# Kernel tuning notes

Hardware: AMD Instinct MI355X
Metric: run time of the kernel (lower is better)

The kernel has to match this reference:

```python
import jax, jax.numpy as jnp
import numpy as np

L, N, E, H, D, F = 2048, 2, 1024, 16, 64, 4096  # seq, batch, embed, heads, head_dim, ffn
EPS = 1e-5


def _ln(x, w, b):
    m = jnp.mean(x, axis=-1, keepdims=True)
    v = jnp.mean(jnp.square(x - m), axis=-1, keepdims=True)
    return (x - m) * jax.lax.rsqrt(v + EPS) * w + b


def setup_inputs() -> dict:
    key = jax.random.key(0)
    ks = jax.random.split(key, 16)
    s = 0.02
    f32 = jnp.float32
    return {
        "x": jax.random.normal(ks[0], (L, N, E), f32),
        "ln1_w": jnp.ones((E,), f32),
        "ln1_b": jnp.zeros((E,), f32),
        "wq": jax.random.normal(ks[1], (H * D, E), f32) * s,
        "bq": jnp.zeros((H * D,), f32),
        "wk": jax.random.normal(ks[2], (H * D, E), f32) * s,
        "bk": jnp.zeros((H * D,), f32),
        "wv": jax.random.normal(ks[3], (H * D, E), f32) * s,
        "bv": jnp.zeros((H * D,), f32),
        "wout": jax.random.normal(ks[4], (E, H * D), f32) * s,
        "bout": jnp.zeros((E,), f32),
        "ln2_w": jnp.ones((E,), f32),
        "ln2_b": jnp.zeros((E,), f32),
        "fc1_w": jax.random.normal(ks[5], (F, E), f32) * s,
        "fc1_b": jnp.zeros((F,), f32),
        "fc2_w": jax.random.normal(ks[6], (E, F), f32) * s,
        "fc2_b": jnp.zeros((E,), f32),
    }


def reference(x, ln1_w, ln1_b, wq, bq, wk, bk, wv, bv, wout, bout,
              ln2_w, ln2_b, fc1_w, fc1_b, fc2_w, fc2_b):
    scale = D ** (-0.5)
    residual = x
    h = _ln(x, ln1_w, ln1_b)                      # (L,N,E)
    q = (h @ wq.T + bq).reshape(L, N, H, D) * scale
    k = (h @ wk.T + bk).reshape(L, N, H, D)
    v = (h @ wv.T + bv).reshape(L, N, H, D)
    attn = jnp.einsum('qnhd,knhd->nhqk', q, k)    # (N,H,L,L) full score matrix
    causal = jnp.tril(jnp.ones((L, L), bool))
    attn = jnp.where(causal[None, None], attn, jnp.float32(-10000.0))
    p = jax.nn.softmax(attn, axis=-1)
    o = jnp.einsum('nhqk,knhd->qnhd', p, v).reshape(L, N, H * D)
    o = o @ wout.T + bout
    x = o + residual
    residual = x
    h = _ln(x, ln2_w, ln2_b)
    h = jax.nn.gelu(h @ fc1_w.T + fc1_b, approximate=False)
    h = h @ fc2_w.T + fc2_b
    return h + residual
```

## Files before the change

### kernel.cpp

```cpp
#include <hip/hip_runtime.h>
#include <hip/hip_bf16.h>
#include <math.h>

using bf16 = __hip_bfloat16;
typedef __bf16 bf16x8 __attribute__((ext_vector_type(8)));
typedef short  short4v __attribute__((ext_vector_type(4)));
typedef float  f32x4  __attribute__((ext_vector_type(4)));

static constexpr int Lq = 2048, Nb = 2, E = 1024, Hh = 16, Dd = 64, Ff = 4096;
static constexpr int MT = Lq * Nb;

__device__ __forceinline__ void async_lds16(const void* g, void* l) {
  __builtin_amdgcn_global_load_lds(
      (const __attribute__((address_space(1))) void*)g,
      (__attribute__((address_space(3))) void*)l, 16, 0, 0);
}
__device__ __forceinline__ bf16x8 ld8(const bf16* p) { return *(const bf16x8*)p; }
__device__ __forceinline__ short bfbits(float x) {
  bf16 t = __float2bfloat16(x);
  return *(short*)&t;
}
__device__ __forceinline__ float gelu_fast(float v) {
  const float y = fminf(2.302208f * (v + 0.044715f * v * v * v), 80.f);
  const float t = exp2f(y);
  return v * t / (t + 1.0f);
}

__global__ __launch_bounds__(256) void cvt_all_kernel(
    const float* __restrict__ wq, const float* __restrict__ wk,
    const float* __restrict__ wv, const float* __restrict__ wout,
    const float* __restrict__ fc1w, const float* __restrict__ fc2w,
    bf16* __restrict__ wqkvb, bf16* __restrict__ woutb,
    bf16* __restrict__ f1wb, bf16* __restrict__ f2wb) {
  const int i = blockIdx.x * 256 + threadIdx.x;
  const float* src;
  bf16* dst;
  size_t off;
  if (i < 786432) {
    const int r = i >> 18;
    off = (size_t)(i & 262143);
    src = (r == 0) ? wq : (r == 1) ? wk : wv;
    dst = wqkvb + (size_t)r * (E * E);
  } else if (i < 1048576) {
    off = (size_t)(i - 786432); src = wout; dst = woutb;
  } else if (i < 2097152) {
    off = (size_t)(i - 1048576); src = fc1w; dst = f1wb;
  } else {
    off = (size_t)(i - 2097152); src = fc2w; dst = f2wb;
  }
  float4 v = ((const float4*)src)[off];
  bf16 o4[4] = {__float2bfloat16(v.x), __float2bfloat16(v.y),
                __float2bfloat16(v.z), __float2bfloat16(v.w)};
  *(uint2*)(dst + 4 * off) = *(uint2*)o4;
}

template <int K, int KSTR, int NOUT, int EPI>
__global__ __launch_bounds__(512, 4) void gemm_tlp(
    const bf16* __restrict__ A, const bf16* __restrict__ W,
    const float* __restrict__ b1, const float* __restrict__ b2,
    const float* __restrict__ b3, float qscale,
    bf16* __restrict__ o0, bf16* __restrict__ o1,
    bf16* __restrict__ o2, bf16* __restrict__ o3) {
  __shared__ __align__(16) bf16 sm[2][12288];
  constexpr int NKT = K / 32;
  static_assert(NKT >= 2, "need >=2 K-tiles");
  const int tid = threadIdx.x;
  const int w = tid >> 6, lane = tid & 63;
  const int quad = lane >> 4, l16 = lane & 15;
  const int wm = (w >> 2) * 64, wn = (w & 3) * 64;
  const int m0 = blockIdx.y * 128, n0 = blockIdx.x * 256;
  const int koff = blockIdx.z * K;

  const int srow = tid >> 2;
  const int sca = ((tid & 3) ^ ((srow >> 1) & 3)) * 8;
  const bf16* Asrc = A + (size_t)(m0 + srow) * KSTR + koff + sca;
  const bf16* Wsrc0 = W + (size_t)(n0 + srow) * KSTR + koff + sca;
  const bf16* Wsrc1 = W + (size_t)(n0 + 128 + srow) * KSTR + koff + sca;
  const int d8 = tid * 8;

  const int kq = ((quad ^ ((l16 >> 1) & 3)) << 3);

  f32x4 acc[4][4];
#pragma unroll
  for (int i = 0; i < 4; i++)
#pragma unroll
    for (int j = 0; j < 4; j++)
#pragma unroll
      for (int r = 0; r < 4; r++) acc[i][j][r] = 0.f;

  async_lds16(Asrc, &sm[0][d8]);
  async_lds16(Wsrc0, &sm[0][4096 + d8]);
  async_lds16(Wsrc1, &sm[0][8192 + d8]);

  for (int kt = 0; kt < NKT; ++kt) {
    const bf16* S = sm[kt & 1];
    if (kt + 1 < NKT) {
      const int kn = (kt + 1) * 32;
      bf16* D = sm[(kt & 1) ^ 1];
      async_lds16(Asrc + kn, &D[d8]);
      async_lds16(Wsrc0 + kn, &D[4096 + d8]);
      async_lds16(Wsrc1 + kn, &D[8192 + d8]);
      asm volatile("s_waitcnt vmcnt(3)" ::: "memory");
    } else {
      asm volatile("s_waitcnt vmcnt(0)" ::: "memory");
    }
    __builtin_amdgcn_s_barrier();

    bf16x8 a[4], b[4];
#pragma unroll
    for (int i = 0; i < 4; i++)
      a[i] = ld8(&S[(wm + i * 16 + l16) * 32 + kq]);
#pragma unroll
    for (int j = 0; j < 4; j++)
      b[j] = ld8(&S[4096 + (wn + j * 16 + l16) * 32 + kq]);

    __builtin_amdgcn_s_setprio(1);
#pragma unroll
    for (int i = 0; i < 4; i++)
#pragma unroll
      for (int j = 0; j < 4; j++)
        acc[i][j] = __builtin_amdgcn_mfma_f32_16x16x32_bf16(a[i], b[j], acc[i][j], 0, 0, 0);
    __builtin_amdgcn_s_setprio(0);
    __builtin_amdgcn_sched_barrier(0);
    __builtin_amdgcn_s_barrier();
  }

  if constexpr (EPI == 2) {
#pragma unroll
    for (int j = 0; j < 4; j++) {
      const int col = n0 + wn + j * 16 + l16;
      const float bv = b1[col];
#pragma unroll
      for (int i = 0; i < 4; i++) {
        const int row = m0 + wm + i * 16 + quad * 4;
#pragma unroll
        for (int r = 0; r < 4; r++) {
          o0[(size_t)(row + r) * NOUT + col] =
              __float2bfloat16(gelu_fast(acc[i][j][r] + bv));
        }
      }
    }
  } else if constexpr (EPI == 3) {
    bf16* dst = (blockIdx.z == 0) ? o0
              : (blockIdx.z == 1) ? o1
              : (blockIdx.z == 2) ? o2 : o3;
#pragma unroll
    for (int j = 0; j < 4; j++) {
      const int col = n0 + wn + j * 16 + l16;
#pragma unroll
      for (int i = 0; i < 4; i++) {
        const int row = m0 + wm + i * 16 + quad * 4;
#pragma unroll
        for (int r = 0; r < 4; r++) {
          dst[(size_t)(row + r) * NOUT + col] = __float2bfloat16(acc[i][j][r]);
        }
      }
    }
  } else {
    const int seg = n0 >> 10;
#pragma unroll
    for (int j = 0; j < 4; j++) {
      const int col = n0 + wn + j * 16 + l16;
      const float bv = (seg == 0) ? b1[col]
                     : (seg == 1) ? b2[col - 1024] : b3[col - 2048];
      const int d = col & 63;
#pragma unroll
      for (int i = 0; i < 4; i++) {
        const int row = m0 + wm + i * 16 + quad * 4;
#pragma unroll
        for (int r = 0; r < 4; r++) {
          const int tok = row + r, n = tok & 1, l = tok >> 1;
          float v = acc[i][j][r] + bv;
          if (seg == 0) {
            o0[(size_t)tok * 1024 + col] = __float2bfloat16(v * qscale);
          } else if (seg == 1) {
            const int h = (col - 1024) >> 6, hh = n * 16 + h;
            o2[((((size_t)hh * 32 + (l >> 6)) * 8 + (d >> 3)) * 64 + (l & 63)) * 8 +
               (d & 7)] = __float2bfloat16(v);
          } else {
            const int h = (col - 2048) >> 6, hh = n * 16 + h;
            o1[((((size_t)hh * 32 + (l >> 6)) * 8 + ((l >> 3) & 7)) * 64 + d) * 8 +
               (l & 7)] = __float2bfloat16(v);
          }
        }
      }
    }
  }
}

__global__ __launch_bounds__(256) void reduce4_kernel(
    const bf16* __restrict__ P0, const bf16* __restrict__ P1,
    const bf16* __restrict__ P2, const bf16* __restrict__ P3,
    const float* __restrict__ bias, float* __restrict__ out) {
  const int i = blockIdx.x * 256 + threadIdx.x;
  const size_t e0 = (size_t)i * 4;
  const int col = (int)(e0 & (E - 1));
  uint2 a0 = *(const uint2*)(P0 + e0);
  uint2 a1 = *(const uint2*)(P1 + e0);
  uint2 a2 = *(const uint2*)(P2 + e0);
  uint2 a3 = *(const uint2*)(P3 + e0);
  const bf16* q0 = (const bf16*)&a0;
  const bf16* q1 = (const bf16*)&a1;
  const bf16* q2 = (const bf16*)&a2;
  const bf16* q3 = (const bf16*)&a3;
  float4 b = *(const float4*)(bias + col);
  float4 r = *(const float4*)(out + e0);
  float4 o;
  o.x = (float)q0[0] + (float)q1[0] + (float)q2[0] + (float)q3[0] + b.x + r.x;
  o.y = (float)q0[1] + (float)q1[1] + (float)q2[1] + (float)q3[1] + b.y + r.y;
  o.z = (float)q0[2] + (float)q1[2] + (float)q2[2] + (float)q3[2] + b.z + r.z;
  o.w = (float)q0[3] + (float)q1[3] + (float)q2[3] + (float)q3[3] + b.w + r.w;
  *(float4*)(out + e0) = o;
}

__global__ __launch_bounds__(256) void redln_kernel(
    const bf16* __restrict__ P, const float* __restrict__ bias,
    const float* __restrict__ res, const float* __restrict__ wgt,
    const float* __restrict__ bia, float* __restrict__ resout,
    bf16* __restrict__ h2) {
  const int t = blockIdx.x, tid = threadIdx.x;
  const size_t base = (size_t)t * E;
  const int e0 = tid * 4;
  uint2 u0 = *(const uint2*)(P + base + e0);
  uint2 u1 = *(const uint2*)(P + (size_t)MT * E + base + e0);
  const bf16* p0 = (const bf16*)&u0;
  const bf16* p1 = (const bf16*)&u1;
  float4 b = *(const float4*)(bias + e0);
  float4 r = *(const float4*)(res + base + e0);
  float v4[4];
  v4[0] = (float)p0[0] + (float)p1[0] + b.x + r.x;
  v4[1] = (float)p0[1] + (float)p1[1] + b.y + r.y;
  v4[2] = (float)p0[2] + (float)p1[2] + b.z + r.z;
  v4[3] = (float)p0[3] + (float)p1[3] + b.w + r.w;
  *(float4*)(resout + base + e0) = *(float4*)v4;

  float s = 0.f, ss = 0.f;
#pragma unroll
  for (int i = 0; i < 4; i++) { s += v4[i]; ss += v4[i] * v4[i]; }
  for (int off = 32; off > 0; off >>= 1) {
    s += __shfl_down(s, off, 64);
    ss += __shfl_down(ss, off, 64);
  }
  __shared__ float rs[4], rss[4], mv[2];
  const int w = tid >> 6;
  if ((tid & 63) == 0) { rs[w] = s; rss[w] = ss; }
  __syncthreads();
  if (tid == 0) {
    float S = rs[0] + rs[1] + rs[2] + rs[3];
    float SS = rss[0] + rss[1] + rss[2] + rss[3];
    float mean = S * (1.f / E);
    float var = SS * (1.f / E) - mean * mean;
    mv[0] = mean; mv[1] = rsqrtf(var + 1e-5f);
  }
  __syncthreads();
  const float mean = mv[0], rstd = mv[1];
  float4 wg = *(const float4*)(wgt + e0);
  float4 bb = *(const float4*)(bia + e0);
  bf16 o4[4];
  o4[0] = __float2bfloat16((v4[0] - mean) * rstd * wg.x + bb.x);
  o4[1] = __float2bfloat16((v4[1] - mean) * rstd * wg.y + bb.y);
  o4[2] = __float2bfloat16((v4[2] - mean) * rstd * wg.z + bb.z);
  o4[3] = __float2bfloat16((v4[3] - mean) * rstd * wg.w + bb.w);
  *(uint2*)(h2 + base + e0) = *(uint2*)o4;
}

__global__ __launch_bounds__(256) void ln_kernel(
    const float* __restrict__ x, const float* __restrict__ wgt,
    const float* __restrict__ bia, bf16* __restrict__ out) {
  const int t = blockIdx.x, tid = threadIdx.x;
  const size_t base = (size_t)t * E;
  float v4[4], s = 0.f, ss = 0.f;
#pragma unroll
  for (int i = 0; i < 4; i++) {
    float v = x[base + i * 256 + tid];
    v4[i] = v; s += v; ss += v * v;
  }
  for (int off = 32; off > 0; off >>= 1) {
    s += __shfl_down(s, off, 64);
    ss += __shfl_down(ss, off, 64);
  }
  __shared__ float rs[4], rss[4], mv[2];
  const int w = tid >> 6;
  if ((tid & 63) == 0) { rs[w] = s; rss[w] = ss; }
  __syncthreads();
  if (tid == 0) {
    float S = rs[0] + rs[1] + rs[2] + rs[3];
    float SS = rss[0] + rss[1] + rss[2] + rss[3];
    float mean = S * (1.f / E);
    float var = SS * (1.f / E) - mean * mean;
    mv[0] = mean; mv[1] = rsqrtf(var + 1e-5f);
  }
  __syncthreads();
  const float mean = mv[0], rstd = mv[1];
#pragma unroll
  for (int i = 0; i < 4; i++) {
    const int e = i * 256 + tid;
    float r = (v4[i] - mean) * rstd * wgt[e] + bia[e];
    out[base + e] = __float2bfloat16(r);
  }
}

__global__ __launch_bounds__(256) void attn_kernel(
    const bf16* __restrict__ Q1, const bf16* __restrict__ KT,
    const bf16* __restrict__ VT, bf16* __restrict__ O) {
  __shared__ __align__(16) bf16 KB[2][512 * 8];
  __shared__ __align__(16) bf16 VB[2][512 * 8];
  const int tid = threadIdx.x;
  const int w = tid >> 6, lane = tid & 63, quad = lane >> 4, l16 = lane & 15;
  const int bid = blockIdx.x;
  const int x = bid & 7;
  const int m = (bid >> 3) & 31;
  const int g = bid >> 8;
  const int j = m >> 2;
  const int hh = (m & 3) * 8 + x;
  const int qt = (g == 0) ? j : (g == 1) ? (31 - j) : (g == 2) ? (j + 8) : (23 - j);
  const int n = hh >> 4, h = hh & 15;

  const bf16* Qp = Q1 + n * E + h * Dd;
  const bf16* Kb = KT + (size_t)hh * 32 * 4096;
  const bf16* Vb = VT + (size_t)hh * 32 * 4096;
  const int so = w * 512 + lane * 8;

  const int ql = qt * 64 + w * 16 + l16;
  const bf16x8 aq0 = ld8(Qp + (size_t)ql * 2048 + quad * 8);
  const bf16x8 aq1 = ld8(Qp + (size_t)ql * 2048 + 32 + quad * 8);
  asm volatile("s_waitcnt vmcnt(0)" ::: "memory");

  async_lds16(Kb + so, &KB[0][w * 512]);
  async_lds16(Kb + 2048 + so, &KB[0][2048 + w * 512]);
  async_lds16(Vb + so, &VB[0][w * 512]);
  async_lds16(Vb + 2048 + so, &VB[0][2048 + w * 512]);

  f32x4 o_acc[4];
#pragma unroll
  for (int d = 0; d < 4; d++)
#pragma unroll
    for (int r = 0; r < 4; r++) o_acc[d][r] = 0.f;
  float m_run = -3e30f, l_run = 0.f;

  for (int kt = 0; kt <= qt; ++kt) {
    const bf16* KBb = KB[kt & 1];
    const bf16* VBb = VB[kt & 1];
    if (kt < qt) {
      const size_t tb = (size_t)(kt + 1) * 4096;
      bf16* Kd = &KB[(kt & 1) ^ 1][0];
      bf16* Vd = &VB[(kt & 1) ^ 1][0];
      async_lds16(Kb + tb + so, Kd + w * 512);
      async_lds16(Kb + tb + 2048 + so, Kd + 2048 + w * 512);
      async_lds16(Vb + tb + so, Vd + w * 512);
      async_lds16(Vb + tb + 2048 + so, Vd + 2048 + w * 512);
      asm volatile("s_waitcnt vmcnt(4)" ::: "memory");
    } else {
      asm volatile("s_waitcnt vmcnt(0)" ::: "memory");
    }
    __builtin_amdgcn_s_barrier();

    f32x4 s[4];
    __builtin_amdgcn_s_setprio(1);
#pragma unroll
    for (int ks = 0; ks < 4; ks++) {
      const bf16x8 kc0 = ld8(&KBb[(size_t)((quad)*64 + ks * 16 + l16) * 8]);
      const bf16x8 kc1 = ld8(&KBb[(size_t)((4 + quad) * 64 + ks * 16 + l16) * 8]);
#pragma unroll
      for (int r = 0; r < 4; r++) s[ks][r] = 0.f;
      s[ks] = __builtin_amdgcn_mfma_f32_16x16x32_bf16(kc0, aq0, s[ks], 0, 0, 0);
      s[ks] = __builtin_amdgcn_mfma_f32_16x16x32_bf16(kc1, aq1, s[ks], 0, 0, 0);
    }
    __builtin_amdgcn_s_setprio(0);

    if (kt == qt) {
#pragma unroll
      for (int ks = 0; ks < 4; ks++) {
#pragma unroll
        for (int r = 0; r < 4; r++) {
          const int kg = kt * 64 + ks * 16 + quad * 4 + r;
          if (kg > ql) s[ks][r] = -14427.0f;
        }
      }
    }

    float tmax = s[0][0];
#pragma unroll
    for (int ks = 0; ks < 4; ks++)
#pragma unroll
      for (int r = 0; r < 4; r++) tmax = fmaxf(tmax, s[ks][r]);
    tmax = fmaxf(tmax, __shfl_xor(tmax, 16, 64));
    tmax = fmaxf(tmax, __shfl_xor(tmax, 32, 64));
    float mbase = m_run;
    if (__any(tmax - m_run > 8.0f)) {
      const float mnew = fmaxf(m_run, tmax);
      const float alpha = exp2f(m_run - mnew);
      m_run = mnew;
      mbase = mnew;
      l_run *= alpha;
#pragma unroll
      for (int d = 0; d < 4; d++)
#pragma unroll
        for (int r = 0; r < 4; r++) o_acc[d][r] *= alpha;
    }
    float rsum = 0.f;
    short4v pf[4];
#pragma unroll
    for (int ks = 0; ks < 4; ks++) {
#pragma unroll
      for (int r = 0; r < 4; r++) {
        const float pv = exp2f(s[ks][r] - mbase);
        rsum += pv;
        pf[ks][r] = bfbits(pv);
      }
    }
    rsum += __shfl_xor(rsum, 16, 64);
    rsum += __shfl_xor(rsum, 32, 64);
    l_run += rsum;

    __builtin_amdgcn_s_setprio(1);
#pragma unroll
    for (int d = 0; d < 4; d++) {
#pragma unroll
      for (int ks = 0; ks < 4; ks++) {
        const int gg = ks * 2 + (quad >> 1);
        const short4v av =
            *(const short4v*)&VBb[(size_t)(gg * 64 + d * 16 + l16) * 8 + (quad & 1) * 4];
        o_acc[d] = __builtin_amdgcn_mfma_f32_16x16x16bf16_1k(av, pf[ks], o_acc[d], 0, 0, 0);
      }
    }
    __builtin_amdgcn_s_setprio(0);

    __builtin_amdgcn_sched_barrier(0);
    __builtin_amdgcn_s_barrier();
  }

  const float inv_l = 1.f / fmaxf(l_run, 1e-30f);
  const size_t obase = (size_t)ql * (Nb * E) + (size_t)n * E + h * Dd;
#pragma unroll
  for (int d = 0; d < 4; d++)
#pragma unroll
    for (int r = 0; r < 4; r++)
      O[obase + d * 16 + quad * 4 + r] = __float2bfloat16(o_acc[d][r] * inv_l);
}

extern "C" void kernel_launch(void* const* d_in, const int* in_sizes, int n_in,
                              void* d_out, int out_size, void* d_ws, size_t ws_size,
                              hipStream_t stream) {
  const float* x    = (const float*)d_in[0];
  const float* ln1w = (const float*)d_in[1];
  const float* ln1b = (const float*)d_in[2];
  const float* wq   = (const float*)d_in[3];
  const float* bq   = (const float*)d_in[4];
  const float* wk   = (const float*)d_in[5];
  const float* bk   = (const float*)d_in[6];
  const float* wv   = (const float*)d_in[7];
  const float* bv   = (const float*)d_in[8];
  const float* wout = (const float*)d_in[9];
  const float* bout = (const float*)d_in[10];
  const float* ln2w = (const float*)d_in[11];
  const float* ln2b = (const float*)d_in[12];
  const float* fc1w = (const float*)d_in[13];
  const float* fc1b = (const float*)d_in[14];
  const float* fc2w = (const float*)d_in[15];
  const float* fc2b = (const float*)d_in[16];

  char* ws = (char*)d_ws;
  bf16* wqkvb = (bf16*)(ws);
  bf16* woutb = (bf16*)(ws + ((size_t)6 << 20));
  bf16* f1wb  = (bf16*)(ws + ((size_t)8 << 20));
  bf16* f2wb  = (bf16*)(ws + ((size_t)16 << 20));
  bf16* h1    = (bf16*)(ws + ((size_t)24 << 20));
  bf16* qk1   = (bf16*)(ws + ((size_t)32 << 20));
  bf16* ktg   = (bf16*)(ws + ((size_t)40 << 20));
  bf16* vtg   = (bf16*)(ws + ((size_t)48 << 20));
  bf16* o     = (bf16*)(ws + ((size_t)56 << 20));
  bf16* Pout  = (bf16*)(ws + ((size_t)32 << 20));
  bf16* f1    = (bf16*)(ws + ((size_t)32 << 20));
  bf16* h2    = h1;
  bf16* FP0   = (bf16*)(ws);
  bf16* FP1   = (bf16*)(ws + ((size_t)8 << 20));
  bf16* FP2   = (bf16*)(ws + ((size_t)64 << 20));
  bf16* FP3   = (bf16*)(ws + ((size_t)72 << 20));
  float* outp = (float*)d_out;

  cvt_all_kernel<<<12288, 256, 0, stream>>>(wq, wk, wv, wout, fc1w, fc2w,
                                            wqkvb, woutb, f1wb, f2wb);

  ln_kernel<<<MT, 256, 0, stream>>>(x, ln1w, ln1b, h1);

  gemm_tlp<1024, 1024, 3072, 4><<<dim3(12, 32), 512, 0, stream>>>(
      h1, wqkvb, bq, bk, bv, 0.125f * 1.44269504f, qk1, vtg, ktg, nullptr);

  attn_kernel<<<1024, 256, 0, stream>>>(qk1, ktg, vtg, o);

  gemm_tlp<512, 1024, 1024, 3><<<dim3(4, 32, 2), 512, 0, stream>>>(
      o, woutb, nullptr, nullptr, nullptr, 1.f,
      Pout, Pout + (size_t)MT * E, nullptr, nullptr);
  redln_kernel<<<MT, 256, 0, stream>>>(Pout, bout, x, ln2w, ln2b, outp, h2);

  gemm_tlp<1024, 1024, 4096, 2><<<dim3(16, 32), 512, 0, stream>>>(
      h2, f1wb, fc1b, nullptr, nullptr, 1.f, f1, nullptr, nullptr, nullptr);

  gemm_tlp<1024, 4096, 1024, 3><<<dim3(4, 32, 4), 512, 0, stream>>>(
      f1, f2wb, nullptr, nullptr, nullptr, 1.f, FP0, FP1, FP2, FP3);
  reduce4_kernel<<<MT * E / 1024, 256, 0, stream>>>(FP0, FP1, FP2, FP3, fc2b, outp);
}
```

Measured before the change: 345.0 us.

## Split attention query tile across two 128-thread blocks, swizzle K layout, drop double-buffering

The attention kernel now runs 2048 blocks of 128 threads, each covering half of a 64-row query tile, instead of 1024 blocks of 256 threads. This gives more, smaller blocks for scheduling and occupancy. The K/V staging changes from double-buffered async prefetch to a single buffer loaded and synchronized every iteration, which exposes load latency but halves LDS use. The K tile is now written by the QKV GEMM epilogue with an XOR swizzle on the token index, and read with the matching swizzle, to reduce LDS bank conflicts. Each K/V tile is also fetched twice as often across blocks.

```diff
diff --git a/kernel.cpp b/kernel.cpp
--- a/kernel.cpp
+++ b/kernel.cpp
@@ -175,8 +175,8 @@
             o0[(size_t)tok * 1024 + col] = __float2bfloat16(v * qscale);
           } else if (seg == 1) {
             const int h = (col - 1024) >> 6, hh = n * 16 + h;
-            o2[((((size_t)hh * 32 + (l >> 6)) * 8 + (d >> 3)) * 64 + (l & 63)) * 8 +
-               (d & 7)] = __float2bfloat16(v);
+            o2[((((size_t)hh * 32 + (l >> 6)) * 8 + (d >> 3)) * 64 +
+                ((l & 63) ^ (d >> 3))) * 8 + (d & 7)] = __float2bfloat16(v);
           } else {
             const int h = (col - 2048) >> 6, hh = n * 16 + h;
             o1[((((size_t)hh * 32 + (l >> 6)) * 8 + ((l >> 3) & 7)) * 64 + d) * 8 +
@@ -300,17 +300,18 @@
   }
 }
 
-__global__ __launch_bounds__(256) void attn_kernel(
+__global__ __launch_bounds__(128) void attn_kernel(
     const bf16* __restrict__ Q1, const bf16* __restrict__ KT,
     const bf16* __restrict__ VT, bf16* __restrict__ O) {
-  __shared__ __align__(16) bf16 KB[2][512 * 8];
-  __shared__ __align__(16) bf16 VB[2][512 * 8];
+  __shared__ __align__(16) bf16 KB[4096];
+  __shared__ __align__(16) bf16 VB[4096];
   const int tid = threadIdx.x;
   const int w = tid >> 6, lane = tid & 63, quad = lane >> 4, l16 = lane & 15;
   const int bid = blockIdx.x;
   const int x = bid & 7;
   const int m = (bid >> 3) & 31;
-  const int g = bid >> 8;
+  const int g = (bid >> 8) & 3;
+  const int half = (bid >> 10) & 1;
   const int j = m >> 2;
   const int hh = (m & 3) * 8 + x;
   const int qt = (g == 0) ? j : (g == 1) ? (31 - j) : (g == 2) ? (j + 8) : (23 - j);
@@ -319,52 +320,39 @@
   const bf16* Qp = Q1 + n * E + h * Dd;
   const bf16* Kb = KT + (size_t)hh * 32 * 4096;
   const bf16* Vb = VT + (size_t)hh * 32 * 4096;
-  const int so = w * 512 + lane * 8;
-
-  const int ql = qt * 64 + w * 16 + l16;
+  const int t8 = tid * 8;
+
+  const int ql = qt * 64 + half * 32 + w * 16 + l16;
   const bf16x8 aq0 = ld8(Qp + (size_t)ql * 2048 + quad * 8);
   const bf16x8 aq1 = ld8(Qp + (size_t)ql * 2048 + 32 + quad * 8);
-  asm volatile("s_waitcnt vmcnt(0)" ::: "memory");
-
-  async_lds16(Kb + so, &KB[0][w * 512]);
-  async_lds16(Kb + 2048 + so, &KB[0][2048 + w * 512]);
-  async_lds16(Vb + so, &VB[0][w * 512]);
-  async_lds16(Vb + 2048 + so, &VB[0][2048 + w * 512]);
 
   f32x4 o_acc[4];
 #pragma unroll
   for (int d = 0; d < 4; d++)
 #pragma unroll
     for (int r = 0; r < 4; r++) o_acc[d][r] = 0.f;
+  const f32x4 z4 = {0.f, 0.f, 0.f, 0.f};
   float m_run = -3e30f, l_run = 0.f;
 
   for (int kt = 0; kt <= qt; ++kt) {
-    const bf16* KBb = KB[kt & 1];
-    const bf16* VBb = VB[kt & 1];
-    if (kt < qt) {
-      const size_t tb = (size_t)(kt + 1) * 4096;
-      bf16* Kd = &KB[(kt & 1) ^ 1][0];
-      bf16* Vd = &VB[(kt & 1) ^ 1][0];
-      async_lds16(Kb + tb + so, Kd + w * 512);
-      async_lds16(Kb + tb + 2048 + so, Kd + 2048 + w * 512);
-      async_lds16(Vb + tb + so, Vd + w * 512);
-      async_lds16(Vb + tb + 2048 + so, Vd + 2048 + w * 512);
-      asm volatile("s_waitcnt vmcnt(4)" ::: "memory");
-    } else {
-      asm volatile("s_waitcnt vmcnt(0)" ::: "memory");
-    }
-    __builtin_amdgcn_s_barrier();
+    const size_t tb = (size_t)kt * 4096;
+#pragma unroll
+    for (int r = 0; r < 4; r++) {
+      async_lds16(Kb + tb + t8 + r * 1024, &KB[t8 + r * 1024]);
+      async_lds16(Vb + tb + t8 + r * 1024, &VB[t8 + r * 1024]);
+    }
+    __syncthreads();
 
     f32x4 s[4];
     __builtin_amdgcn_s_setprio(1);
 #pragma unroll
     for (int ks = 0; ks < 4; ks++) {
-      const bf16x8 kc0 = ld8(&KBb[(size_t)((quad)*64 + ks * 16 + l16) * 8]);
-      const bf16x8 kc1 = ld8(&KBb[(size_t)((4 + quad) * 64 + ks * 16 + l16) * 8]);
-#pragma unroll
-      for (int r = 0; r < 4; r++) s[ks][r] = 0.f;
-      s[ks] = __builtin_amdgcn_mfma_f32_16x16x32_bf16(kc0, aq0, s[ks], 0, 0, 0);
-      s[ks] = __builtin_amdgcn_mfma_f32_16x16x32_bf16(kc1, aq1, s[ks], 0, 0, 0);
+      const int tok = ks * 16 + l16;
+      const bf16x8 kc0 = ld8(&KB[(size_t)(quad * 64 + (tok ^ quad)) * 8]);
+      const bf16x8 kc1 = ld8(&KB[(size_t)((4 + quad) * 64 + (tok ^ (4 + quad))) * 8]);
+      s[ks] = __builtin_amdgcn_mfma_f32_16x16x32_bf16(
+          kc1, aq1,
+          __builtin_amdgcn_mfma_f32_16x16x32_bf16(kc0, aq0, z4, 0, 0, 0), 0, 0, 0);
     }
     __builtin_amdgcn_s_setprio(0);
 
@@ -379,11 +367,11 @@
       }
     }
 
-    float tmax = s[0][0];
-#pragma unroll
-    for (int ks = 0; ks < 4; ks++)
-#pragma unroll
-      for (int r = 0; r < 4; r++) tmax = fmaxf(tmax, s[ks][r]);
+    float tmax = fmaxf(fmaxf(fmaxf(s[0][0], s[0][1]), fmaxf(s[0][2], s[0][3])),
+                       fmaxf(fmaxf(s[1][0], s[1][1]), fmaxf(s[1][2], s[1][3])));
+    tmax = fmaxf(tmax,
+                 fmaxf(fmaxf(fmaxf(s[2][0], s[2][1]), fmaxf(s[2][2], s[2][3])),
+                       fmaxf(fmaxf(s[3][0], s[3][1]), fmaxf(s[3][2], s[3][3]))));
     tmax = fmaxf(tmax, __shfl_xor(tmax, 16, 64));
     tmax = fmaxf(tmax, __shfl_xor(tmax, 32, 64));
     float mbase = m_run;
@@ -420,14 +408,13 @@
       for (int ks = 0; ks < 4; ks++) {
         const int gg = ks * 2 + (quad >> 1);
         const short4v av =
-            *(const short4v*)&VBb[(size_t)(gg * 64 + d * 16 + l16) * 8 + (quad & 1) * 4];
+            *(const short4v*)&VB[(size_t)(gg * 64 + d * 16 + l16) * 8 + (quad & 1) * 4];
         o_acc[d] = __builtin_amdgcn_mfma_f32_16x16x16bf16_1k(av, pf[ks], o_acc[d], 0, 0, 0);
       }
     }
     __builtin_amdgcn_s_setprio(0);
 
-    __builtin_amdgcn_sched_barrier(0);
-    __builtin_amdgcn_s_barrier();
+    __syncthreads();
   }
 
   const float inv_l = 1.f / fmaxf(l_run, 1e-30f);
@@ -487,7 +474,7 @@
   gemm_tlp<1024, 1024, 3072, 4><<<dim3(12, 32), 512, 0, stream>>>(
       h1, wqkvb, bq, bk, bv, 0.125f * 1.44269504f, qk1, vtg, ktg, nullptr);
 
-  attn_kernel<<<1024, 256, 0, stream>>>(qk1, ktg, vtg, o);
+  attn_kernel<<<2048, 128, 0, stream>>>(qk1, ktg, vtg, o);
 
   gemm_tlp<512, 1024, 1024, 3><<<dim3(4, 32, 2), 512, 0, stream>>>(
       o, woutb, nullptr, nullptr, nullptr, 1.f,
```

Result: slower. 357.8 us (+3.7%).

## Swizzle K tile layout in attention and split out-projection K four ways

Applied to the files above, without the earlier changes.

The K tile written by the QKV GEMM epilogue now XORs the token index with the head-dim chunk, and the attention kernel reads it back with the same XOR. This is meant to cut LDS bank conflicts on the K fragment loads. Separately, the output-projection GEMM now splits its reduction dimension four ways instead of two to launch more blocks. The fused reduce-plus-LayerNorm kernel therefore sums four bf16 partials, which adds partial-buffer traffic and one more bf16 rounding step.

```diff
diff --git a/kernel.cpp b/kernel.cpp
--- a/kernel.cpp
+++ b/kernel.cpp
@@ -175,8 +175,8 @@
             o0[(size_t)tok * 1024 + col] = __float2bfloat16(v * qscale);
           } else if (seg == 1) {
             const int h = (col - 1024) >> 6, hh = n * 16 + h;
-            o2[((((size_t)hh * 32 + (l >> 6)) * 8 + (d >> 3)) * 64 + (l & 63)) * 8 +
-               (d & 7)] = __float2bfloat16(v);
+            o2[((((size_t)hh * 32 + (l >> 6)) * 8 + (d >> 3)) * 64 +
+                ((l & 63) ^ (d >> 3))) * 8 + (d & 7)] = __float2bfloat16(v);
           } else {
             const int h = (col - 2048) >> 6, hh = n * 16 + h;
             o1[((((size_t)hh * 32 + (l >> 6)) * 8 + ((l >> 3) & 7)) * 64 + d) * 8 +
@@ -214,24 +214,30 @@
 }
 
 __global__ __launch_bounds__(256) void redln_kernel(
-    const bf16* __restrict__ P, const float* __restrict__ bias,
-    const float* __restrict__ res, const float* __restrict__ wgt,
-    const float* __restrict__ bia, float* __restrict__ resout,
-    bf16* __restrict__ h2) {
+    const bf16* __restrict__ P0, const bf16* __restrict__ P1,
+    const bf16* __restrict__ P2, const bf16* __restrict__ P3,
+    const float* __restrict__ bias, const float* __restrict__ res,
+    const float* __restrict__ wgt, const float* __restrict__ bia,
+    float* __restrict__ resout, bf16* __restrict__ h2) {
   const int t = blockIdx.x, tid = threadIdx.x;
   const size_t base = (size_t)t * E;
   const int e0 = tid * 4;
-  uint2 u0 = *(const uint2*)(P + base + e0);
-  uint2 u1 = *(const uint2*)(P + (size_t)MT * E + base + e0);
+  uint2 u0 = *(const uint2*)(P0 + base + e0);
+  uint2 u1 = *(const uint2*)(P1 + base + e0);
+  uint2 u2 = *(const uint2*)(P2 + base + e0);
+  uint2 u3 = *(const uint2*)(P3 + base + e0);
   const bf16* p0 = (const bf16*)&u0;
   const bf16* p1 = (const bf16*)&u1;
+  const bf16* p2 = (const bf16*)&u2;
+  const bf16* p3 = (const bf16*)&u3;
   float4 b = *(const float4*)(bias + e0);
   float4 r = *(const float4*)(res + base + e0);
   float v4[4];
-  v4[0] = (float)p0[0] + (float)p1[0] + b.x + r.x;
-  v4[1] = (float)p0[1] + (float)p1[1] + b.y + r.y;
-  v4[2] = (float)p0[2] + (float)p1[2] + b.z + r.z;
-  v4[3] = (float)p0[3] + (float)p1[3] + b.w + r.w;
+#pragma unroll
+  for (int i = 0; i < 4; i++) {
+    v4[i] = (float)p0[i] + (float)p1[i] + (float)p2[i] + (float)p3[i] +
+            ((const float*)&b)[i] + ((const float*)&r)[i];
+  }
   *(float4*)(resout + base + e0) = *(float4*)v4;
 
   float s = 0.f, ss = 0.f;
@@ -336,6 +342,7 @@
   for (int d = 0; d < 4; d++)
 #pragma unroll
     for (int r = 0; r < 4; r++) o_acc[d][r] = 0.f;
+  const f32x4 z4 = {0.f, 0.f, 0.f, 0.f};
   float m_run = -3e30f, l_run = 0.f;
 
   for (int kt = 0; kt <= qt; ++kt) {
@@ -359,12 +366,12 @@
     __builtin_amdgcn_s_setprio(1);
 #pragma unroll
     for (int ks = 0; ks < 4; ks++) {
-      const bf16x8 kc0 = ld8(&KBb[(size_t)((quad)*64 + ks * 16 + l16) * 8]);
-      const bf16x8 kc1 = ld8(&KBb[(size_t)((4 + quad) * 64 + ks * 16 + l16) * 8]);
-#pragma unroll
-      for (int r = 0; r < 4; r++) s[ks][r] = 0.f;
-      s[ks] = __builtin_amdgcn_mfma_f32_16x16x32_bf16(kc0, aq0, s[ks], 0, 0, 0);
-      s[ks] = __builtin_amdgcn_mfma_f32_16x16x32_bf16(kc1, aq1, s[ks], 0, 0, 0);
+      const int tok = ks * 16 + l16;
+      const bf16x8 kc0 = ld8(&KBb[(size_t)(quad * 64 + (tok ^ quad)) * 8]);
+      const bf16x8 kc1 = ld8(&KBb[(size_t)((4 + quad) * 64 + (tok ^ (4 + quad))) * 8]);
+      s[ks] = __builtin_amdgcn_mfma_f32_16x16x32_bf16(
+          kc1, aq1,
+          __builtin_amdgcn_mfma_f32_16x16x32_bf16(kc0, aq0, z4, 0, 0, 0), 0, 0, 0);
     }
     __builtin_amdgcn_s_setprio(0);
 
@@ -470,7 +477,10 @@
   bf16* ktg   = (bf16*)(ws + ((size_t)40 << 20));
   bf16* vtg   = (bf16*)(ws + ((size_t)48 << 20));
   bf16* o     = (bf16*)(ws + ((size_t)56 << 20));
-  bf16* Pout  = (bf16*)(ws + ((size_t)32 << 20));
+  bf16* OP0   = (bf16*)(ws + ((size_t)32 << 20));
+  bf16* OP1   = (bf16*)(ws + ((size_t)40 << 20));
+  bf16* OP2   = (bf16*)(ws + ((size_t)48 << 20));
+  bf16* OP3   = (bf16*)(ws + ((size_t)64 << 20));
   bf16* f1    = (bf16*)(ws + ((size_t)32 << 20));
   bf16* h2    = h1;
   bf16* FP0   = (bf16*)(ws);
@@ -489,10 +499,10 @@
 
   attn_kernel<<<1024, 256, 0, stream>>>(qk1, ktg, vtg, o);
 
-  gemm_tlp<512, 1024, 1024, 3><<<dim3(4, 32, 2), 512, 0, stream>>>(
-      o, woutb, nullptr, nullptr, nullptr, 1.f,
-      Pout, Pout + (size_t)MT * E, nullptr, nullptr);
-  redln_kernel<<<MT, 256, 0, stream>>>(Pout, bout, x, ln2w, ln2b, outp, h2);
+  gemm_tlp<256, 1024, 1024, 3><<<dim3(4, 32, 4), 512, 0, stream>>>(
+      o, woutb, nullptr, nullptr, nullptr, 1.f, OP0, OP1, OP2, OP3);
+  redln_kernel<<<MT, 256, 0, stream>>>(OP0, OP1, OP2, OP3, bout, x, ln2w, ln2b,
+                                       outp, h2);
 
   gemm_tlp<1024, 1024, 4096, 2><<<dim3(16, 32), 512, 0, stream>>>(
       h2, f1wb, fc1b, nullptr, nullptr, 1.f, f1, nullptr, nullptr, nullptr);
```

Result: slower. 364.1 us (+5.5%).
